# Kernel optimization log

Hardware: AMD Instinct MI355X
Metric: run time of the kernel (lower is better)

The kernel has to match this reference:

```python
import jax, jax.numpy as jnp
import numpy as np


def setup_inputs() -> dict:
    key = jax.random.key(0)
    k1, k2, k3 = jax.random.split(key, 3)
    bs, n1, n2, d1, d2, dout = 4, 128, 128, 768, 768, 768
    input1 = jax.random.normal(k1, (bs, n1, d1), dtype=jnp.float32)
    input2 = jax.random.normal(k2, (bs, n2, d2), dtype=jnp.float32)
    # torch Linear(sum_dims, dout): we store W as (d1+d2, dout) so y = x @ W + b
    W = jax.random.normal(k3, (d1 + d2, dout), dtype=jnp.float32) * (1.0 / np.sqrt(d1 + d2))
    b = jnp.zeros((dout,), dtype=jnp.float32)
    return {"input1": input1, "input2": input2, "W": W, "b": b}


def reference(input1, input2, W, b):
    # Original: expand to [bs,n1,n2,d1]/[bs,n1,n2,d2], cat -> [bs,n1,n2,d1+d2], Linear.
    # Algebraically identical without materializing the concat:
    #   cat([x1,x2]) @ W = x1 @ W[:d1] + x2 @ W[d1:]
    d1 = input1.shape[-1]
    W1, W2 = W[:d1], W[d1:]
    p1 = jnp.einsum("bnd,do->bno", input1, W1)  # [bs, n1, dout]
    p2 = jnp.einsum("bmd,do->bmo", input2, W2)  # [bs, n2, dout]
    # broadcast-sum over the pair grid -> [bs, n1, n2, dout]
    return p1[:, :, None, :] + p2[:, None, :, :] + b
```

## Files before the change

### kernel.cpp

```cpp
#include <hip/hip_runtime.h>

#define BM 64
#define BN 64
#define BK 16

__global__ __launch_bounds__(256) void gemm_kernel(
    const float* __restrict__ A1, const float* __restrict__ A2,
    const float* __restrict__ W, const float* __restrict__ bias,
    float* __restrict__ P)
{
    __shared__ float As[BK][BM + 4];
    __shared__ float Bs[BK][BN + 4];

    const int z  = blockIdx.z;
    const int n0 = blockIdx.x * BN;
    const int m0 = blockIdx.y * BM;
    const int t  = threadIdx.x;

    const float* A = z ? A2 : A1;
    const int wrow0 = z * 768;

    const int a_m = t >> 2;
    const int a_k = (t & 3) * 4;
    const int b_k = t >> 4;
    const int b_n = (t & 15) * 4;

    const int tm = (t >> 4) * 4;
    const int tn = (t & 15) * 4;

    float acc[4][4] = {};

    for (int k0 = 0; k0 < 768; k0 += BK) {
        float4 av = *(const float4*)(A + (m0 + a_m) * 768 + k0 + a_k);
        float4 bv = *(const float4*)(W + (wrow0 + k0 + b_k) * 768 + n0 + b_n);
        __syncthreads();
        As[a_k + 0][a_m] = av.x;
        As[a_k + 1][a_m] = av.y;
        As[a_k + 2][a_m] = av.z;
        As[a_k + 3][a_m] = av.w;
        *(float4*)&Bs[b_k][b_n] = bv;
        __syncthreads();
        #pragma unroll
        for (int k = 0; k < BK; ++k) {
            const float4 a4 = *(const float4*)&As[k][tm];
            const float4 b4 = *(const float4*)&Bs[k][tn];
            const float ar[4] = {a4.x, a4.y, a4.z, a4.w};
            const float br[4] = {b4.x, b4.y, b4.z, b4.w};
            #pragma unroll
            for (int i = 0; i < 4; ++i)
                #pragma unroll
                for (int j = 0; j < 4; ++j)
                    acc[i][j] += ar[i] * br[j];
        }
    }

    float4 bb = make_float4(0.f, 0.f, 0.f, 0.f);
    if (z) bb = *(const float4*)(bias + n0 + tn);

    #pragma unroll
    for (int i = 0; i < 4; ++i) {
        const int gm = z * 512 + m0 + tm + i;
        float4 r;
        r.x = acc[i][0] + bb.x;
        r.y = acc[i][1] + bb.y;
        r.z = acc[i][2] + bb.z;
        r.w = acc[i][3] + bb.w;
        *(float4*)(P + (size_t)gm * 768 + n0 + tn) = r;
    }
}

__global__ __launch_bounds__(192) void bcast_kernel(
    const float* __restrict__ P, float* __restrict__ out)
{
    const int t     = threadIdx.x;
    const int bn    = blockIdx.x;
    const int b     = bn >> 7;
    const int mbase = blockIdx.y * 32;

    const float4 p1v = *(const float4*)(P + (size_t)bn * 768 + t * 4);
    const float* p2base = P + (size_t)(512 + b * 128) * 768;
    float* obase = out + (size_t)bn * (128 * 768);

    #pragma unroll 4
    for (int mm = 0; mm < 32; ++mm) {
        const int m = mbase + mm;
        const float4 p2v = *(const float4*)(p2base + (size_t)m * 768 + t * 4);
        float4 r;
        r.x = p1v.x + p2v.x;
        r.y = p1v.y + p2v.y;
        r.z = p1v.z + p2v.z;
        r.w = p1v.w + p2v.w;
        *(float4*)(obase + (size_t)m * 768 + t * 4) = r;
    }
}

extern "C" void kernel_launch(void* const* d_in, const int* in_sizes, int n_in,
                              void* d_out, int out_size, void* d_ws, size_t ws_size,
                              hipStream_t stream)
{
    const float* input1 = (const float*)d_in[0];
    const float* input2 = (const float*)d_in[1];
    const float* W      = (const float*)d_in[2];
    const float* bias   = (const float*)d_in[3];
    float* out = (float*)d_out;
    float* P   = (float*)d_ws;

    dim3 gblock(256);
    dim3 ggrid(768 / BN, 512 / BM, 2);
    gemm_kernel<<<ggrid, gblock, 0, stream>>>(input1, input2, W, bias, P);

    dim3 wblock(192);
    dim3 wgrid(512, 4);
    bcast_kernel<<<wgrid, wblock, 0, stream>>>(P, out);
}
```

Measured before the change: 283.9 us.

## Split-K the projection GEMM, double-buffer LDS, nontemporal broadcast stores

Splits the K dimension of the small projection GEMM in two, doubling the block count so more CUs are busy, and folds the two partial sums together inside the broadcast kernel. Adds register prefetch with double-buffered shared memory so each iteration needs one barrier instead of two. The broadcast kernel now writes the large output with nontemporal stores and unrolls further. The cost is extra partial-sum reads in the bandwidth-bound broadcast, and the split path only runs when the workspace is large enough.

```diff
diff --git a/kernel.cpp b/kernel.cpp
--- a/kernel.cpp
+++ b/kernel.cpp
@@ -4,21 +4,26 @@
 #define BN 64
 #define BK 16
 
+typedef float f4 __attribute__((ext_vector_type(4)));
+
+template<int KS>
 __global__ __launch_bounds__(256) void gemm_kernel(
     const float* __restrict__ A1, const float* __restrict__ A2,
     const float* __restrict__ W, const float* __restrict__ bias,
     float* __restrict__ P)
 {
-    __shared__ float As[BK][BM + 4];
-    __shared__ float Bs[BK][BN + 4];
+    constexpr int KLEN = 768 / KS;
+    __shared__ float As[2][BK][BM + 4];
+    __shared__ float Bs[2][BK][BN + 4];
 
-    const int z  = blockIdx.z;
+    const int bz = blockIdx.z;
+    const int z  = bz & 1;
+    const int ks = bz >> 1;
     const int n0 = blockIdx.x * BN;
     const int m0 = blockIdx.y * BM;
     const int t  = threadIdx.x;
 
     const float* A = z ? A2 : A1;
-    const int wrow0 = z * 768;
 
     const int a_m = t >> 2;
     const int a_k = (t & 3) * 4;
@@ -28,22 +33,31 @@
     const int tm = (t >> 4) * 4;
     const int tn = (t & 15) * 4;
 
+    const float* Aptr = A + (size_t)(m0 + a_m) * 768 + ks * KLEN + a_k;
+    const float* Bptr = W + (size_t)(z * 768 + ks * KLEN + b_k) * 768 + n0 + b_n;
+
+    float4 av = *(const float4*)Aptr;
+    float4 bv = *(const float4*)Bptr;
+
     float acc[4][4] = {};
+    int cur = 0;
 
-    for (int k0 = 0; k0 < 768; k0 += BK) {
-        float4 av = *(const float4*)(A + (m0 + a_m) * 768 + k0 + a_k);
-        float4 bv = *(const float4*)(W + (wrow0 + k0 + b_k) * 768 + n0 + b_n);
-        __syncthreads();
-        As[a_k + 0][a_m] = av.x;
-        As[a_k + 1][a_m] = av.y;
-        As[a_k + 2][a_m] = av.z;
-        As[a_k + 3][a_m] = av.w;
-        *(float4*)&Bs[b_k][b_n] = bv;
+    #pragma unroll 2
+    for (int k0 = 0; k0 < KLEN; k0 += BK) {
+        As[cur][a_k + 0][a_m] = av.x;
+        As[cur][a_k + 1][a_m] = av.y;
+        As[cur][a_k + 2][a_m] = av.z;
+        As[cur][a_k + 3][a_m] = av.w;
+        *(float4*)&Bs[cur][b_k][b_n] = bv;
+        if (k0 + BK < KLEN) {
+            av = *(const float4*)(Aptr + (k0 + BK));
+            bv = *(const float4*)(Bptr + (size_t)(k0 + BK) * 768);
+        }
         __syncthreads();
         #pragma unroll
         for (int k = 0; k < BK; ++k) {
-            const float4 a4 = *(const float4*)&As[k][tm];
-            const float4 b4 = *(const float4*)&Bs[k][tn];
+            const float4 a4 = *(const float4*)&As[cur][k][tm];
+            const float4 b4 = *(const float4*)&Bs[cur][k][tn];
             const float ar[4] = {a4.x, a4.y, a4.z, a4.w};
             const float br[4] = {b4.x, b4.y, b4.z, b4.w};
             #pragma unroll
@@ -52,23 +66,25 @@
                 for (int j = 0; j < 4; ++j)
                     acc[i][j] += ar[i] * br[j];
         }
+        cur ^= 1;
     }
 
     float4 bb = make_float4(0.f, 0.f, 0.f, 0.f);
-    if (z) bb = *(const float4*)(bias + n0 + tn);
+    if (z == 1 && ks == 0) bb = *(const float4*)(bias + n0 + tn);
 
+    const int prow0 = ks * 1024 + z * 512 + m0 + tm;
     #pragma unroll
     for (int i = 0; i < 4; ++i) {
-        const int gm = z * 512 + m0 + tm + i;
         float4 r;
         r.x = acc[i][0] + bb.x;
         r.y = acc[i][1] + bb.y;
         r.z = acc[i][2] + bb.z;
         r.w = acc[i][3] + bb.w;
-        *(float4*)(P + (size_t)gm * 768 + n0 + tn) = r;
+        *(float4*)(P + (size_t)(prow0 + i) * 768 + n0 + tn) = r;
     }
 }
 
+template<int KS>
 __global__ __launch_bounds__(192) void bcast_kernel(
     const float* __restrict__ P, float* __restrict__ out)
 {
@@ -77,20 +93,19 @@
     const int b     = bn >> 7;
     const int mbase = blockIdx.y * 32;
 
-    const float4 p1v = *(const float4*)(P + (size_t)bn * 768 + t * 4);
-    const float* p2base = P + (size_t)(512 + b * 128) * 768;
-    float* obase = out + (size_t)bn * (128 * 768);
+    f4 p1v = *(const f4*)(P + (size_t)bn * 768 + t * 4);
+    if (KS == 2) p1v += *(const f4*)(P + (size_t)(1024 + bn) * 768 + t * 4);
 
-    #pragma unroll 4
+    const float* p2a = P + (size_t)(512 + b * 128) * 768 + t * 4;
+    const float* p2b = P + (size_t)(1536 + b * 128) * 768 + t * 4;
+    float* obase = out + (size_t)bn * (128 * 768) + t * 4;
+
+    #pragma unroll 8
     for (int mm = 0; mm < 32; ++mm) {
         const int m = mbase + mm;
-        const float4 p2v = *(const float4*)(p2base + (size_t)m * 768 + t * 4);
-        float4 r;
-        r.x = p1v.x + p2v.x;
-        r.y = p1v.y + p2v.y;
-        r.z = p1v.z + p2v.z;
-        r.w = p1v.w + p2v.w;
-        *(float4*)(obase + (size_t)m * 768 + t * 4) = r;
+        f4 v = p1v + *(const f4*)(p2a + (size_t)m * 768);
+        if (KS == 2) v += *(const f4*)(p2b + (size_t)m * 768);
+        __builtin_nontemporal_store(v, (f4*)(obase + (size_t)m * 768));
     }
 }
 
@@ -105,11 +120,15 @@
     float* out = (float*)d_out;
     float* P   = (float*)d_ws;
 
-    dim3 gblock(256);
-    dim3 ggrid(768 / BN, 512 / BM, 2);
-    gemm_kernel<<<ggrid, gblock, 0, stream>>>(input1, input2, W, bias, P);
+    const bool split = ws_size >= (size_t)2048 * 768 * sizeof(float);
 
-    dim3 wblock(192);
-    dim3 wgrid(512, 4);
-    bcast_kernel<<<wgrid, wblock, 0, stream>>>(P, out);
+    if (split) {
+        gemm_kernel<2><<<dim3(768 / BN, 512 / BM, 4), 256, 0, stream>>>(
+            input1, input2, W, bias, P);
+        bcast_kernel<2><<<dim3(512, 4), 192, 0, stream>>>(P, out);
+    } else {
+        gemm_kernel<1><<<dim3(768 / BN, 512 / BM, 2), 256, 0, stream>>>(
+            input1, input2, W, bias, P);
+        bcast_kernel<1><<<dim3(512, 4), 192, 0, stream>>>(P, out);
+    }
 }
```

New measurement: 241.5 us. 1.18x faster.

## Fuse projection GEMMs with pairwise broadcast-add into a single kernel

Applied to the files above, without the earlier changes.

Replaces the two-kernel flow (GEMM into a workspace, then broadcast-add) with one kernel. Each block computes a 64x64 tile of both p1 and p2 for one output-column slice using double-buffered shared memory. It then writes the 64x64 pair grid directly with nontemporal stores. This removes the intermediate workspace round-trip and one launch, at the cost of redundant GEMM recomputation across blocks and only 192 blocks to drive the output writes.

```diff
diff --git a/kernel.cpp b/kernel.cpp
--- a/kernel.cpp
+++ b/kernel.cpp
@@ -1,96 +1,114 @@
 #include <hip/hip_runtime.h>
 
-#define BM 64
-#define BN 64
+typedef float f4 __attribute__((ext_vector_type(4)));
+
 #define BK 16
+#define TN 64
+#define TO 64
+#define NTILES 48
 
-__global__ __launch_bounds__(256) void gemm_kernel(
+__global__ __launch_bounds__(256) void fused_kernel(
     const float* __restrict__ A1, const float* __restrict__ A2,
     const float* __restrict__ W, const float* __restrict__ bias,
-    float* __restrict__ P)
+    float* __restrict__ out)
 {
-    __shared__ float As[BK][BM + 4];
-    __shared__ float Bs[BK][BN + 4];
+    __shared__ union {
+        float stage[2][4][BK][TN + 4];
+        float pp2[TN][TO + 4];
+    } u;
 
-    const int z  = blockIdx.z;
-    const int n0 = blockIdx.x * BN;
-    const int m0 = blockIdx.y * BM;
+    const int o0 = blockIdx.x * TO;
+    const int nm = blockIdx.y;
+    const int b  = nm >> 2;
+    const int n0 = ((nm >> 1) & 1) * TN;
+    const int m0 = (nm & 1) * TN;
     const int t  = threadIdx.x;
 
-    const float* A = z ? A2 : A1;
-    const int wrow0 = z * 768;
+    const int ln  = t >> 2;
+    const int lk4 = (t & 3) * 4;
+    const int wk  = t >> 4;
+    const int wo4 = (t & 15) * 4;
 
-    const int a_m = t >> 2;
-    const int a_k = (t & 3) * 4;
-    const int b_k = t >> 4;
-    const int b_n = (t & 15) * 4;
+    const float* a1p = A1 + (size_t)(b * 128 + n0 + ln) * 768 + lk4;
+    const float* a2p = A2 + (size_t)(b * 128 + m0 + ln) * 768 + lk4;
+    const float* w1p = W + (size_t)wk * 768 + o0 + wo4;
+    const float* w2p = W + (size_t)(768 + wk) * 768 + o0 + wo4;
 
-    const int tm = (t >> 4) * 4;
-    const int tn = (t & 15) * 4;
+    const int tr = t >> 4;
+    const int tc = t & 15;
 
-    float acc[4][4] = {};
+    f4 a1v = *(const f4*)(a1p);
+    f4 a2v = *(const f4*)(a2p);
+    f4 w1v = *(const f4*)(w1p);
+    f4 w2v = *(const f4*)(w2p);
+    #pragma unroll
+    for (int i = 0; i < 4; ++i) {
+        u.stage[0][0][lk4 + i][ln] = a1v[i];
+        u.stage[0][1][lk4 + i][ln] = a2v[i];
+    }
+    *(f4*)&u.stage[0][2][wk][wo4] = w1v;
+    *(f4*)&u.stage[0][3][wk][wo4] = w2v;
+    __syncthreads();
 
-    for (int k0 = 0; k0 < 768; k0 += BK) {
-        float4 av = *(const float4*)(A + (m0 + a_m) * 768 + k0 + a_k);
-        float4 bv = *(const float4*)(W + (wrow0 + k0 + b_k) * 768 + n0 + b_n);
-        __syncthreads();
-        As[a_k + 0][a_m] = av.x;
-        As[a_k + 1][a_m] = av.y;
-        As[a_k + 2][a_m] = av.z;
-        As[a_k + 3][a_m] = av.w;
-        *(float4*)&Bs[b_k][b_n] = bv;
-        __syncthreads();
+    f4 acc1[4] = {};
+    f4 acc2[4] = {};
+    int cur = 0;
+
+    for (int tt = 0; tt < NTILES; ++tt) {
+        if (tt + 1 < NTILES) {
+            const int k0 = (tt + 1) * BK;
+            a1v = *(const f4*)(a1p + k0);
+            a2v = *(const f4*)(a2p + k0);
+            w1v = *(const f4*)(w1p + (size_t)k0 * 768);
+            w2v = *(const f4*)(w2p + (size_t)k0 * 768);
+        }
         #pragma unroll
         for (int k = 0; k < BK; ++k) {
-            const float4 a4 = *(const float4*)&As[k][tm];
-            const float4 b4 = *(const float4*)&Bs[k][tn];
-            const float ar[4] = {a4.x, a4.y, a4.z, a4.w};
-            const float br[4] = {b4.x, b4.y, b4.z, b4.w};
+            const f4 x1 = *(const f4*)&u.stage[cur][0][k][tr * 4];
+            const f4 x2 = *(const f4*)&u.stage[cur][1][k][tr * 4];
+            const f4 y1 = *(const f4*)&u.stage[cur][2][k][tc * 4];
+            const f4 y2 = *(const f4*)&u.stage[cur][3][k][tc * 4];
             #pragma unroll
-            for (int i = 0; i < 4; ++i)
-                #pragma unroll
-                for (int j = 0; j < 4; ++j)
-                    acc[i][j] += ar[i] * br[j];
+            for (int i = 0; i < 4; ++i) {
+                acc1[i] += x1[i] * y1;
+                acc2[i] += x2[i] * y2;
+            }
         }
+        if (tt + 1 < NTILES) {
+            const int nxt = cur ^ 1;
+            #pragma unroll
+            for (int i = 0; i < 4; ++i) {
+                u.stage[nxt][0][lk4 + i][ln] = a1v[i];
+                u.stage[nxt][1][lk4 + i][ln] = a2v[i];
+            }
+            *(f4*)&u.stage[nxt][2][wk][wo4] = w1v;
+            *(f4*)&u.stage[nxt][3][wk][wo4] = w2v;
+            __syncthreads();
+        }
+        cur ^= 1;
     }
-
-    float4 bb = make_float4(0.f, 0.f, 0.f, 0.f);
-    if (z) bb = *(const float4*)(bias + n0 + tn);
+    __syncthreads();
 
     #pragma unroll
-    for (int i = 0; i < 4; ++i) {
-        const int gm = z * 512 + m0 + tm + i;
-        float4 r;
-        r.x = acc[i][0] + bb.x;
-        r.y = acc[i][1] + bb.y;
-        r.z = acc[i][2] + bb.z;
-        r.w = acc[i][3] + bb.w;
-        *(float4*)(P + (size_t)gm * 768 + n0 + tn) = r;
-    }
-}
+    for (int i = 0; i < 4; ++i)
+        *(f4*)&u.pp2[tr * 4 + i][tc * 4] = acc2[i];
+    __syncthreads();
 
-__global__ __launch_bounds__(192) void bcast_kernel(
-    const float* __restrict__ P, float* __restrict__ out)
-{
-    const int t     = threadIdx.x;
-    const int bn    = blockIdx.x;
-    const int b     = bn >> 7;
-    const int mbase = blockIdx.y * 32;
+    const f4 bb = *(const f4*)(bias + o0 + tc * 4);
+    f4 p1b[4];
+    #pragma unroll
+    for (int i = 0; i < 4; ++i)
+        p1b[i] = acc1[i] + bb;
 
-    const float4 p1v = *(const float4*)(P + (size_t)bn * 768 + t * 4);
-    const float* p2base = P + (size_t)(512 + b * 128) * 768;
-    float* obase = out + (size_t)bn * (128 * 768);
+    float* ob = out + ((size_t)(b * 128 + n0 + tr * 4) * 128 + m0) * 768 + o0 + tc * 4;
 
     #pragma unroll 4
-    for (int mm = 0; mm < 32; ++mm) {
-        const int m = mbase + mm;
-        const float4 p2v = *(const float4*)(p2base + (size_t)m * 768 + t * 4);
-        float4 r;
-        r.x = p1v.x + p2v.x;
-        r.y = p1v.y + p2v.y;
-        r.z = p1v.z + p2v.z;
-        r.w = p1v.w + p2v.w;
-        *(float4*)(obase + (size_t)m * 768 + t * 4) = r;
+    for (int m = 0; m < TN; ++m) {
+        const f4 p2v = *(const f4*)&u.pp2[m][tc * 4];
+        #pragma unroll
+        for (int i = 0; i < 4; ++i)
+            __builtin_nontemporal_store(p1b[i] + p2v,
+                (f4*)(ob + (size_t)i * 128 * 768 + (size_t)m * 768));
     }
 }
 
@@ -103,13 +121,6 @@
     const float* W      = (const float*)d_in[2];
     const float* bias   = (const float*)d_in[3];
     float* out = (float*)d_out;
-    float* P   = (float*)d_ws;
 
-    dim3 gblock(256);
-    dim3 ggrid(768 / BN, 512 / BM, 2);
-    gemm_kernel<<<ggrid, gblock, 0, stream>>>(input1, input2, W, bias, P);
-
-    dim3 wblock(192);
-    dim3 wgrid(512, 4);
-    bcast_kernel<<<wgrid, wblock, 0, stream>>>(P, out);
+    fused_kernel<<<dim3(768 / TO, 16), 256, 0, stream>>>(input1, input2, W, bias, out);
 }
```

Measured after the change: 303.5 us. 6.9% more time.
